# Performance work log

Hardware: AMD Instinct MI355X
Metric: run time of the kernel (lower is better)

Reference implementation:

```python
import jax, jax.numpy as jnp
import numpy as np
from jax import lax

B, T, N, H, NC = 2, 8, 512, 64, 10
NEG = -1e9
LN_EPS = 1e-5


def _gatv2(x, mask, Wl, Wr, att, b):
    # GATv2Conv (PyG semantics, eval mode): e_ij = att . leaky_relu(Wr x_i + Wl x_j),
    # softmax over source nodes j with self-loops, out_i = sum_j alpha_ij * (Wl x_j).
    # x: (B, N, Fin); mask: (N, N) bool adjacency incl. self-loops; att: (heads, C).
    heads, C = att.shape
    Bn, Nn, _ = x.shape
    xl = (x @ Wl).reshape(Bn, Nn, heads, C)  # source transform
    xr = (x @ Wr).reshape(Bn, Nn, heads, C)  # target transform
    s = jax.nn.leaky_relu(xr[:, :, None] + xl[:, None, :], 0.2)  # (B, Ni, Nj, h, C)
    e = jnp.einsum('bijhc,hc->bijh', s, att)
    e = jnp.where(mask[None, :, :, None], e, NEG)
    alpha = jax.nn.softmax(e, axis=2)  # softmax over neighbors j
    out = jnp.einsum('bijh,bjhc->bihc', alpha, xl)
    return out.reshape(Bn, Nn, heads * C) + b


def _gru_layer(x, Wih, Whh, bih, bhh):
    # torch nn.GRU single layer, batch_first; x: (B, T, Hin)
    h0 = jnp.zeros((x.shape[0], Whh.shape[0]), x.dtype)
    def step(h, xt):
        gi = xt @ Wih + bih
        gh = h @ Whh + bhh
        ir, iz, inn = jnp.split(gi, 3, axis=-1)
        hr, hz, hn = jnp.split(gh, 3, axis=-1)
        r = jax.nn.sigmoid(ir + hr)
        z = jax.nn.sigmoid(iz + hz)
        n = jnp.tanh(inn + r * hn)
        hnew = (1.0 - z) * n + z * h
        return hnew, hnew
    _, ys = lax.scan(step, h0, jnp.swapaxes(x, 0, 1))
    return jnp.swapaxes(ys, 0, 1)


def setup_inputs() -> dict:
    key = jax.random.key(0)
    ks = jax.random.split(key, 20)
    def rn(i, shape, s=0.1):
        return jax.random.normal(ks[i], shape, jnp.float32) * s
    x_seq = jax.random.normal(ks[0], (B, T, N, 1), jnp.float32)
    a = jax.random.uniform(ks[1], (N, N))
    up = jnp.triu((a > 0.95).astype(jnp.float32), 1)
    static_adj = up + up.T  # sparse symmetric 0/1 static graph
    dyn_W = jax.random.normal(ks[2], (N, N), jnp.float32)
    reg_lambda = jnp.array([0.05], jnp.float32)
    return {
        'x_seq': x_seq, 'static_adj': static_adj, 'dyn_W': dyn_W, 'reg_lambda': reg_lambda,
        'g1_Wl': rn(3, (1, H)), 'g1_Wr': rn(4, (1, H)), 'g1_att': rn(5, (4, H // 4)), 'g1_b': jnp.zeros(H),
        'g2_Wl': rn(6, (H, H)), 'g2_Wr': rn(7, (H, H)), 'g2_att': rn(8, (1, H)), 'g2_b': jnp.zeros(H),
        'gru_Wih0': rn(9, (H, 3 * H)), 'gru_Whh0': rn(10, (H, 3 * H)), 'gru_bih0': jnp.zeros(3 * H), 'gru_bhh0': jnp.zeros(3 * H),
        'gru_Wih1': rn(11, (H, 3 * H)), 'gru_Whh1': rn(12, (H, 3 * H)), 'gru_bih1': jnp.zeros(3 * H), 'gru_bhh1': jnp.zeros(3 * H),
        'attn_W': rn(13, (H, 1)), 'attn_b': jnp.zeros(1),
        'cls_W1': rn(14, (H, H)), 'cls_b1': jnp.zeros(H), 'ln_g': jnp.ones(H), 'ln_b': jnp.zeros(H),
        'cls_W2': rn(15, (H, NC)), 'cls_b2': jnp.zeros(NC),
    }


def reference(x_seq, static_adj, dyn_W, reg_lambda,
              g1_Wl, g1_Wr, g1_att, g1_b, g2_Wl, g2_Wr, g2_att, g2_b,
              gru_Wih0, gru_Whh0, gru_bih0, gru_bhh0,
              gru_Wih1, gru_Whh1, gru_bih1, gru_bhh1,
              attn_W, attn_b, cls_W1, cls_b1, ln_g, ln_b, cls_W2, cls_b2):
    Bn, Tn, Nn, _ = x_seq.shape
    lam = jnp.maximum(reg_lambda[0], 0.01)
    t = jnp.arange(Tn, dtype=x_seq.dtype)
    gts = jnp.exp(-lam * t)  # gating values per timestep
    dyn = jax.nn.relu(dyn_W + dyn_W.T)
    fused = gts[:, None, None] * static_adj + (1.0 - gts)[:, None, None] * dyn  # (T, N, N)
    masks = (fused > 0) | jnp.eye(Nn, dtype=bool)[None]  # edge set + self-loops

    def step(carry, inp):
        xt, mask = inp  # xt: (B, N, 1)
        h = jax.nn.elu(_gatv2(xt, mask, g1_Wl, g1_Wr, g1_att, g1_b))
        h = jax.nn.elu(_gatv2(h, mask, g2_Wl, g2_Wr, g2_att, g2_b))
        return carry, h.mean(axis=1)  # (B, H) graph readout

    _, reps = lax.scan(step, 0.0, (jnp.swapaxes(x_seq, 0, 1), masks))
    h_seq = jnp.swapaxes(reps, 0, 1)  # (B, T, H)

    gru_out = _gru_layer(h_seq, gru_Wih0, gru_Whh0, gru_bih0, gru_bhh0)
    gru_out = _gru_layer(gru_out, gru_Wih1, gru_Whh1, gru_bih1, gru_bhh1)

    att_scores = jax.nn.softmax((gru_out @ attn_W + attn_b)[..., 0], axis=1)  # (B, T)
    final = jnp.einsum('bt,bth->bh', att_scores, gru_out)

    z = final @ cls_W1 + cls_b1
    mu = jnp.mean(z, axis=-1, keepdims=True)
    var = jnp.var(z, axis=-1, keepdims=True)
    z = (z - mu) / jnp.sqrt(var + LN_EPS) * ln_g + ln_b
    z = jax.nn.gelu(z, approximate=False)
    logits = z @ cls_W2 + cls_b2
    return logits, gts, att_scores
```

## Files before the change

### kernel.cpp

```cpp
#include <hip/hip_runtime.h>
#include <math.h>

#define BB 2
#define TT 8
#define NN 512
#define HH 64
#define NC 10

typedef unsigned char uchar;

__device__ __forceinline__ float elu1(float v){ return v > 0.f ? v : expm1f(v); }
__device__ __forceinline__ float sigm(float v){ return 1.f/(1.f+expf(-v)); }

__global__ __launch_bounds__(256) void k_mask(
    const float* __restrict__ dW, const float* __restrict__ sadj,
    uchar* __restrict__ M0, uchar* __restrict__ M1,
    float* __restrict__ Z2, float* __restrict__ hseq,
    const float* __restrict__ att1, const float* __restrict__ Wr1,
    const float* __restrict__ Wl1, float* __restrict__ AB)
{
    __shared__ float tr[64][65];
    int bx = blockIdx.x, by = blockIdx.y;
    int i0 = by*64, j0 = bx*64;
    int tid = threadIdx.x;
    #pragma unroll
    for (int q = 0; q < 4; ++q){
        int r = (tid >> 4) + 16*q, c4 = tid & 15;
        float4 v = *(const float4*)&dW[(size_t)(j0+r)*NN + i0 + 4*c4];
        tr[r][4*c4+0] = v.x; tr[r][4*c4+1] = v.y;
        tr[r][4*c4+2] = v.z; tr[r][4*c4+3] = v.w;
    }
    __syncthreads();
    #pragma unroll
    for (int q = 0; q < 4; ++q){
        int row = (tid >> 4) + 16*q, c4 = tid & 15;
        int i = i0 + row, j = j0 + 4*c4;
        float4 d  = *(const float4*)&dW[(size_t)i*NN + j];
        float4 sa = *(const float4*)&sadj[(size_t)i*NN + j];
        uchar4 m0, m1;
        float dd0 = d.x + tr[4*c4+0][row];
        float dd1 = d.y + tr[4*c4+1][row];
        float dd2 = d.z + tr[4*c4+2][row];
        float dd3 = d.w + tr[4*c4+3][row];
        m0.x = (sa.x > 0.f) || (i == j+0);
        m0.y = (sa.y > 0.f) || (i == j+1);
        m0.z = (sa.z > 0.f) || (i == j+2);
        m0.w = (sa.w > 0.f) || (i == j+3);
        m1.x = m0.x || (dd0 > 0.f);
        m1.y = m0.y || (dd1 > 0.f);
        m1.z = m0.z || (dd2 > 0.f);
        m1.w = m0.w || (dd3 > 0.f);
        *(uchar4*)&M0[(size_t)i*NN + j] = m0;
        *(uchar4*)&M1[(size_t)i*NN + j] = m1;
    }
    int flat = (by*8 + bx)*256 + tid;
    if (flat < BB*TT*NN) Z2[flat] = 0.f;
    else if (flat < BB*TT*NN + BB*TT*HH) hseq[flat - BB*TT*NN] = 0.f;
    if (bx == 0 && by == 0 && tid < 8){
        int h = tid & 3;
        const float* W = (tid < 4) ? Wr1 : Wl1;
        float s = 0.f;
        for (int c = 0; c < 16; ++c) s += att1[h*16+c]*W[h*16+c];
        AB[tid] = s;
    }
}

__global__ __launch_bounds__(256) void k_gat1f(
    const float* __restrict__ x_seq, const uchar* __restrict__ M0,
    const uchar* __restrict__ M1,
    const float* __restrict__ Wl, const float* __restrict__ Wr,
    const float* __restrict__ att, const float* __restrict__ bias,
    const float* __restrict__ AB,
    const float* __restrict__ Wl2, const float* __restrict__ Wr2,
    const float* __restrict__ att2,
    float* __restrict__ xl2, float* __restrict__ xr2,
    float* __restrict__ ui, float* __restrict__ vj)
{
    __shared__ float x_s[NN];
    __shared__ float S_s[4][4];
    __shared__ float h_s[4][HH];
    __shared__ float Wl2_s[64*64];
    __shared__ float Wr2_s[64*64];
    int bt = blockIdx.y; int t = bt % TT;
    int i0 = blockIdx.x * 4;
    int tid = threadIdx.x;
    int il = tid >> 6, jl = tid & 63;
    int i = i0 + il;
    const uchar* M = t ? M1 : M0;
    ((float2*)x_s)[tid] = ((const float2*)(x_seq + bt*NN))[tid];
    #pragma unroll
    for (int q = 0; q < 4; ++q){
        int idx = q*256 + tid;
        ((float4*)Wl2_s)[idx] = ((const float4*)Wl2)[idx];
        ((float4*)Wr2_s)[idx] = ((const float4*)Wr2)[idx];
    }
    __syncthreads();
    float xi = x_s[i];
    const uchar* Mrow = M + (size_t)i*NN;
    float xj[8], msk[8];
    #pragma unroll
    for (int jj = 0; jj < 8; ++jj){
        int j = jj*64 + jl;
        xj[jj] = x_s[j];
        msk[jj] = Mrow[j] ? 1.f : 0.f;
    }
    float sw[4] = {0,0,0,0}, swx[4] = {0,0,0,0};
    for (int h = 0; h < 4; ++h){
        float acc[8] = {0,0,0,0,0,0,0,0};
        #pragma unroll
        for (int c = 0; c < 16; ++c){
            int hc = h*16 + c;
            float wl = Wl[hc];
            float q  = 0.4f * att[hc];
            float pr = xi * Wr[hc];
            #pragma unroll
            for (int jj = 0; jj < 8; ++jj){
                float s = fmaf(xj[jj], wl, pr);
                acc[jj] = fmaf(q, fabsf(s), acc[jj]);
            }
        }
        float lin = 0.6f * xi * AB[h];
        float al6 = 0.6f * AB[4+h];
        #pragma unroll
        for (int jj = 0; jj < 8; ++jj){
            float e = acc[jj] + fmaf(al6, xj[jj], lin);
            float w = msk[jj] * __expf(e);
            sw[h] += w;
            swx[h] = fmaf(w, xj[jj], swx[h]);
        }
    }
    #pragma unroll
    for (int off = 32; off; off >>= 1){
        #pragma unroll
        for (int h = 0; h < 4; ++h){
            sw[h]  += __shfl_down(sw[h],  off);
            swx[h] += __shfl_down(swx[h], off);
        }
    }
    if (jl == 0){
        #pragma unroll
        for (int h = 0; h < 4; ++h) S_s[il][h] = swx[h] / sw[h];
    }
    __syncthreads();
    {
        int hc = tid & 63, row = tid >> 6;
        float v = S_s[row][hc >> 4] * Wl[hc] + bias[hc];
        h_s[row][hc] = elu1(v);
    }
    __syncthreads();
    {
        int c = tid & 63, row = tid >> 6;
        float al = 0.f, ar = 0.f;
        #pragma unroll 8
        for (int k = 0; k < 64; ++k){
            float hv = h_s[row][k];
            al = fmaf(hv, Wl2_s[k*64 + c], al);
            ar = fmaf(hv, Wr2_s[k*64 + c], ar);
        }
        size_t ridx = (size_t)(bt*NN + i0 + row);
        xl2[ridx*HH + c] = al;
        xr2[ridx*HH + c] = ar;
        float a2 = att2[c];
        float pu = a2 * ar, pv = a2 * al;
        #pragma unroll
        for (int off = 32; off; off >>= 1){
            pu += __shfl_down(pu, off);
            pv += __shfl_down(pv, off);
        }
        if (c == 0){ ui[ridx] = pu; vj[ridx] = pv; }
    }
}

__global__ __launch_bounds__(256) void k_e2(
    const float* __restrict__ xl2, const float* __restrict__ xr2,
    const uchar* __restrict__ M0, const uchar* __restrict__ M1,
    const float* __restrict__ att,
    const float* __restrict__ ui, const float* __restrict__ vj,
    float* __restrict__ WgT, float* __restrict__ Z2)
{
    __shared__ float xrT[64][68];
    __shared__ float xlT[64][68];
    int bt = blockIdx.z, t = bt % TT;
    int i0 = blockIdx.y*64, j0 = blockIdx.x*64;
    int base = bt*NN;
    int tid = threadIdx.x;
    const uchar* M = t ? M1 : M0;
    {
        int r = tid >> 2;
        #pragma unroll
        for (int q = 0; q < 4; ++q){
            int c4 = (tid & 3) + 4*q;
            float4 a = *(const float4*)&xr2[(size_t)(base+i0+r)*HH + 4*c4];
            float4 b = *(const float4*)&xl2[(size_t)(base+j0+r)*HH + 4*c4];
            xrT[4*c4+0][r] = a.x; xrT[4*c4+1][r] = a.y;
            xrT[4*c4+2][r] = a.z; xrT[4*c4+3][r] = a.w;
            xlT[4*c4+0][r] = b.x; xlT[4*c4+1][r] = b.y;
            xlT[4*c4+2][r] = b.z; xlT[4*c4+3][r] = b.w;
        }
    }
    int ti = tid >> 4, tj = tid & 15;
    int iL = ti*4, jL = tj*4;
    float4 u4 = *(const float4*)&ui[base+i0+iL];
    float4 v4 = *(const float4*)&vj[base+j0+jL];
    float uu[4] = {u4.x, u4.y, u4.z, u4.w};
    float vv[4] = {v4.x, v4.y, v4.z, v4.w};
    float acc[4][4];
    #pragma unroll
    for (int ii = 0; ii < 4; ++ii)
        #pragma unroll
        for (int jj = 0; jj < 4; ++jj)
            acc[ii][jj] = 0.6f*(uu[ii] + vv[jj]);
    __syncthreads();
    #pragma unroll 8
    for (int c = 0; c < 64; ++c){
        float qa = 0.4f * att[c];
        float4 a4 = *(const float4*)&xrT[c][iL];
        float4 b4 = *(const float4*)&xlT[c][jL];
        float a[4] = {a4.x, a4.y, a4.z, a4.w};
        float b[4] = {b4.x, b4.y, b4.z, b4.w};
        #pragma unroll
        for (int ii = 0; ii < 4; ++ii)
            #pragma unroll
            for (int jj = 0; jj < 4; ++jj)
                acc[ii][jj] = fmaf(qa, fabsf(a[ii] + b[jj]), acc[ii][jj]);
    }
    float w[4][4];
    #pragma unroll
    for (int ii = 0; ii < 4; ++ii){
        int i = i0 + iL + ii;
        uchar4 mr = *(const uchar4*)&M[(size_t)i*NN + j0 + jL];
        w[ii][0] = mr.x ? __expf(acc[ii][0]) : 0.f;
        w[ii][1] = mr.y ? __expf(acc[ii][1]) : 0.f;
        w[ii][2] = mr.z ? __expf(acc[ii][2]) : 0.f;
        w[ii][3] = mr.w ? __expf(acc[ii][3]) : 0.f;
    }
    #pragma unroll
    for (int jj = 0; jj < 4; ++jj){
        int j = j0 + jL + jj;
        float4 wv = { w[0][jj], w[1][jj], w[2][jj], w[3][jj] };
        *(float4*)&WgT[(size_t)(base+j)*NN + i0 + iL] = wv;
    }
    #pragma unroll
    for (int ii = 0; ii < 4; ++ii){
        float zi = w[ii][0] + w[ii][1] + w[ii][2] + w[ii][3];
        zi += __shfl_down(zi, 8);
        zi += __shfl_down(zi, 4);
        zi += __shfl_down(zi, 2);
        zi += __shfl_down(zi, 1);
        if (tj == 0) atomicAdd(&Z2[base + i0 + iL + ii], zi);
    }
}

__global__ __launch_bounds__(256) void k_a2(
    const float* __restrict__ WgT, const float* __restrict__ xl2,
    const float* __restrict__ Z2, const float* __restrict__ bias,
    float* __restrict__ hseq)
{
    __shared__ float a_s[64][20];
    __shared__ float x_s[64][68];
    __shared__ float msum[64];
    int bt = blockIdx.y;
    int i0 = blockIdx.x * 16;
    int base = bt * NN;
    int tid = threadIdx.x;
    int tg = tid >> 4, tc = tid & 15;
    if (tid < 64) msum[tid] = 0.f;
    float4 acc = {0,0,0,0};
    for (int jc = 0; jc < 8; ++jc){
        int j0 = jc*64;
        {
            int row = tid >> 2, c4 = tid & 3;
            ((float4*)&a_s[row][0])[c4] = ((const float4*)&WgT[(size_t)(base+j0+row)*NN + i0])[c4];
        }
        #pragma unroll
        for (int q = 0; q < 4; ++q){
            int idx = q*256 + tid; int row = idx >> 4, c4 = idx & 15;
            ((float4*)&x_s[row][0])[c4] = ((const float4*)&xl2[(size_t)(base+j0+row)*HH])[c4];
        }
        __syncthreads();
        #pragma unroll 8
        for (int j = 0; j < 64; ++j){
            float a = a_s[j][tg];
            float4 xv = ((float4*)&x_s[j][0])[tc];
            acc.x = fmaf(a, xv.x, acc.x);
            acc.y = fmaf(a, xv.y, acc.y);
            acc.z = fmaf(a, xv.z, acc.z);
            acc.w = fmaf(a, xv.w, acc.w);
        }
        __syncthreads();
    }
    float rz = 1.f / Z2[base + i0 + tg];
    float4 b4 = ((const float4*)bias)[tc];
    float4 h;
    h.x = elu1(acc.x*rz + b4.x);
    h.y = elu1(acc.y*rz + b4.y);
    h.z = elu1(acc.z*rz + b4.z);
    h.w = elu1(acc.w*rz + b4.w);
    atomicAdd(&msum[tc*4+0], h.x);
    atomicAdd(&msum[tc*4+1], h.y);
    atomicAdd(&msum[tc*4+2], h.z);
    atomicAdd(&msum[tc*4+3], h.w);
    __syncthreads();
    if (tid < 64) atomicAdd(&hseq[bt*HH + tid], msum[tid]*(1.f/(float)NN));
}

__global__ __launch_bounds__(512) void k_gruhead(
    const float* __restrict__ hseq,
    const float* __restrict__ Wih0, const float* __restrict__ Whh0,
    const float* __restrict__ bih0, const float* __restrict__ bhh0,
    const float* __restrict__ Wih1, const float* __restrict__ Whh1,
    const float* __restrict__ bih1, const float* __restrict__ bhh1,
    const float* __restrict__ lamp, const float* __restrict__ attn_W,
    const float* __restrict__ attn_b, const float* __restrict__ W1,
    const float* __restrict__ b1, const float* __restrict__ ln_g,
    const float* __restrict__ ln_b, const float* __restrict__ W2,
    const float* __restrict__ b2, float* __restrict__ out)
{
    __shared__ float W_s[64*192];
    __shared__ float gi_s[BB*TT*192];
    __shared__ float x_s[BB*TT*HH];
    __shared__ float y_s[BB*TT*HH];
    __shared__ float h_s[BB][HH];
    __shared__ float gh_s[BB][192];
    __shared__ float sc_s[BB][TT], at_s[BB][TT];
    __shared__ float fin_s[BB][HH], z_s[BB][HH], g_s[BB][HH];
    __shared__ float mu_s[BB], iv_s[BB];
    int tid = threadIdx.x;
    int b = tid / 192, g = tid % 192;
    for (int k = tid; k < BB*TT*HH; k += 512) x_s[k] = hseq[k];
    for (int L = 0; L < 2; ++L){
        const float* Wih = L ? Wih1 : Wih0;
        const float* Whh = L ? Whh1 : Whh0;
        const float* bih = L ? bih1 : bih0;
        const float* bhh = L ? bhh1 : bhh0;
        __syncthreads();
        for (int k = tid; k < 64*192; k += 512) W_s[k] = Wih[k];
        __syncthreads();
        if (tid < 384){
            float accT[TT];
            #pragma unroll
            for (int t = 0; t < TT; ++t) accT[t] = bih[g];
            for (int k = 0; k < HH; ++k){
                float wk = W_s[k*192 + g];
                #pragma unroll
                for (int t = 0; t < TT; ++t)
                    accT[t] = fmaf(x_s[(b*TT+t)*HH + k], wk, accT[t]);
            }
            #pragma unroll
            for (int t = 0; t < TT; ++t) gi_s[(b*TT+t)*192 + g] = accT[t];
        }
        __syncthreads();
        for (int k = tid; k < 64*192; k += 512) W_s[k] = Whh[k];
        if (tid < BB*HH) h_s[tid>>6][tid&63] = 0.f;
        __syncthreads();
        for (int t = 0; t < TT; ++t){
            if (tid < 384){
                float gh = bhh[g];
                #pragma unroll 8
                for (int k = 0; k < HH; ++k)
                    gh = fmaf(h_s[b][k], W_s[k*192 + g], gh);
                gh_s[b][g] = gh;
            }
            __syncthreads();
            if (tid < BB*HH){
                int b2 = tid >> 6, gg = tid & 63;
                const float* gi = &gi_s[(b2*TT+t)*192];
                float r = sigm(gi[gg]      + gh_s[b2][gg]);
                float z = sigm(gi[64+gg]   + gh_s[b2][64+gg]);
                float n = tanhf(gi[128+gg] + r*gh_s[b2][128+gg]);
                float hn = (1.f - z)*n + z*h_s[b2][gg];
                h_s[b2][gg] = hn;
                y_s[(b2*TT + t)*HH + gg] = hn;
            }
            __syncthreads();
        }
        if (L == 0){
            for (int k = tid; k < BB*TT*HH; k += 512) x_s[k] = y_s[k];
        }
    }
    __syncthreads();
    float lam = fmaxf(lamp[0], 0.01f);
    if (tid < TT) out[BB*NC + tid] = expf(-lam*(float)tid);
    if (tid < BB*TT){
        int bb = tid >> 3, t = tid & 7;
        float s = attn_b[0];
        const float* r = &y_s[(bb*TT+t)*HH];
        for (int h = 0; h < HH; ++h) s += r[h]*attn_W[h];
        sc_s[bb][t] = s;
    }
    __syncthreads();
    if (tid < BB){
        float mx = -INFINITY;
        for (int t = 0; t < TT; ++t) mx = fmaxf(mx, sc_s[tid][t]);
        float se = 0.f;
        for (int t = 0; t < TT; ++t){ float w = expf(sc_s[tid][t]-mx); at_s[tid][t] = w; se += w; }
        for (int t = 0; t < TT; ++t){
            at_s[tid][t] /= se;
            out[BB*NC + TT + tid*TT + t] = at_s[tid][t];
        }
    }
    __syncthreads();
    if (tid < BB*HH){
        int bb = tid >> 6, h = tid & 63;
        float a = 0.f;
        for (int t = 0; t < TT; ++t) a += at_s[bb][t]*y_s[(bb*TT+t)*HH + h];
        fin_s[bb][h] = a;
    }
    __syncthreads();
    if (tid < BB*HH){
        int bb = tid >> 6, h = tid & 63;
        float a = b1[h];
        for (int k = 0; k < HH; ++k) a += fin_s[bb][k]*W1[k*HH+h];
        z_s[bb][h] = a;
    }
    __syncthreads();
    if (tid < BB){
        float mu = 0.f;
        for (int h = 0; h < HH; ++h) mu += z_s[tid][h];
        mu *= (1.f/HH);
        float v = 0.f;
        for (int h = 0; h < HH; ++h){ float d = z_s[tid][h]-mu; v += d*d; }
        v *= (1.f/HH);
        mu_s[tid] = mu; iv_s[tid] = 1.f/sqrtf(v + 1e-5f);
    }
    __syncthreads();
    if (tid < BB*HH){
        int bb = tid >> 6, h = tid & 63;
        float zn = (z_s[bb][h]-mu_s[bb])*iv_s[bb]*ln_g[h] + ln_b[h];
        g_s[bb][h] = 0.5f*zn*(1.f + erff(zn*0.70710678118654752f));
    }
    __syncthreads();
    if (tid < BB*NC){
        int bb = tid / NC, c = tid % NC;
        float a = b2[c];
        for (int k = 0; k < HH; ++k) a += g_s[bb][k]*W2[k*NC+c];
        out[bb*NC + c] = a;
    }
}

extern "C" void kernel_launch(void* const* d_in, const int* in_sizes, int n_in,
                              void* d_out, int out_size, void* d_ws, size_t ws_size,
                              hipStream_t stream)
{
    const float* x_seq = (const float*)d_in[0];
    const float* sadj  = (const float*)d_in[1];
    const float* dynW  = (const float*)d_in[2];
    const float* lamp  = (const float*)d_in[3];
    const float* g1_Wl = (const float*)d_in[4];
    const float* g1_Wr = (const float*)d_in[5];
    const float* g1_att= (const float*)d_in[6];
    const float* g1_b  = (const float*)d_in[7];
    const float* g2_Wl = (const float*)d_in[8];
    const float* g2_Wr = (const float*)d_in[9];
    const float* g2_att= (const float*)d_in[10];
    const float* g2_b  = (const float*)d_in[11];
    const float* Wih0  = (const float*)d_in[12];
    const float* Whh0  = (const float*)d_in[13];
    const float* bih0  = (const float*)d_in[14];
    const float* bhh0  = (const float*)d_in[15];
    const float* Wih1  = (const float*)d_in[16];
    const float* Whh1  = (const float*)d_in[17];
    const float* bih1  = (const float*)d_in[18];
    const float* bhh1  = (const float*)d_in[19];
    const float* attnW = (const float*)d_in[20];
    const float* attnb = (const float*)d_in[21];
    const float* W1    = (const float*)d_in[22];
    const float* b1    = (const float*)d_in[23];
    const float* lng   = (const float*)d_in[24];
    const float* lnb   = (const float*)d_in[25];
    const float* W2    = (const float*)d_in[26];
    const float* b2    = (const float*)d_in[27];
    float* out = (float*)d_out;

    const int RWS = BB*TT*NN*HH;
    uchar* M0 = (uchar*)d_ws;
    uchar* M1 = M0 + (size_t)NN*NN;
    float* fb = (float*)(M1 + (size_t)NN*NN);
    float* Z2   = fb;
    float* AB   = Z2   + BB*TT*NN;
    float* ui   = AB   + 16;
    float* vj   = ui   + BB*TT*NN;
    float* xl2  = vj   + BB*TT*NN;
    float* xr2  = xl2  + RWS;
    float* WgT  = xr2  + RWS;
    float* hseq = WgT  + (size_t)BB*TT*NN*NN;

    k_mask <<<dim3(8,8), 256, 0, stream>>>(dynW, sadj, M0, M1, Z2, hseq, g1_att, g1_Wr, g1_Wl, AB);
    k_gat1f<<<dim3(NN/4, BB*TT), 256, 0, stream>>>(x_seq, M0, M1, g1_Wl, g1_Wr, g1_att, g1_b, AB,
                                                   g2_Wl, g2_Wr, g2_att, xl2, xr2, ui, vj);
    k_e2   <<<dim3(NN/64, NN/64, BB*TT), 256, 0, stream>>>(xl2, xr2, M0, M1, g2_att, ui, vj, WgT, Z2);
    k_a2   <<<dim3(NN/16, BB*TT), 256, 0, stream>>>(WgT, xl2, Z2, g2_b, hseq);
    k_gruhead<<<1, 512, 0, stream>>>(hseq, Wih0, Whh0, bih0, bhh0, Wih1, Whh1, bih1, bhh1,
                                     lamp, attnW, attnb, W1, b1, lng, lnb, W2, b2, out);
}
```

Measured before the change: 226.1 us.

## Restructure GRU head into wave-level recurrence with shuffles and pre-transposed weights

The GRU weights are pre-transposed into gate-interleaved float4 layout inside extra blocks of the mask kernel. The layer-0 input projection moves to a separate small multi-block kernel. The recurrence now runs with one wave per batch element, keeping hidden state in registers and broadcasting it with shuffles, which removes the per-timestep block barriers and shared round trips. This adds an extra kernel launch and uses only two waves for the serial part, leaving most of the block idle.

Measured after the change: 223.0 us. Within noise of the previous version (-1.4%).

```diff
diff --git a/kernel.cpp b/kernel.cpp
--- a/kernel.cpp
+++ b/kernel.cpp
@@ -17,12 +17,29 @@
     uchar* __restrict__ M0, uchar* __restrict__ M1,
     float* __restrict__ Z2, float* __restrict__ hseq,
     const float* __restrict__ att1, const float* __restrict__ Wr1,
-    const float* __restrict__ Wl1, float* __restrict__ AB)
+    const float* __restrict__ Wl1, float* __restrict__ AB,
+    const float* __restrict__ Whh0, const float* __restrict__ Wih1,
+    const float* __restrict__ Whh1, float4* __restrict__ WT4)
 {
     __shared__ float tr[64][65];
     int bx = blockIdx.x, by = blockIdx.y;
+    int tid = threadIdx.x;
+    if (blockIdx.z == 1){
+        int idx = (by*8 + bx)*256 + tid;
+        if (idx < 3*4096){
+            int m = idx >> 12, r = idx & 4095;
+            int gg = r >> 6, k = r & 63;
+            const float* W = (m == 0) ? Whh0 : (m == 1) ? Wih1 : Whh1;
+            float4 o;
+            o.x = W[k*192 + gg];
+            o.y = W[k*192 + 64 + gg];
+            o.z = W[k*192 + 128 + gg];
+            o.w = 0.f;
+            WT4[(size_t)m*4096 + r] = o;
+        }
+        return;
+    }
     int i0 = by*64, j0 = bx*64;
-    int tid = threadIdx.x;
     #pragma unroll
     for (int q = 0; q < 4; ++q){
         int r = (tid >> 4) + 16*q, c4 = tid & 15;
@@ -304,11 +321,24 @@
     if (tid < 64) atomicAdd(&hseq[bt*HH + tid], msum[tid]*(1.f/(float)NN));
 }
 
-__global__ __launch_bounds__(512) void k_gruhead(
-    const float* __restrict__ hseq,
-    const float* __restrict__ Wih0, const float* __restrict__ Whh0,
-    const float* __restrict__ bih0, const float* __restrict__ bhh0,
-    const float* __restrict__ Wih1, const float* __restrict__ Whh1,
+__global__ __launch_bounds__(256) void k_pre(
+    const float* __restrict__ hseq, const float* __restrict__ Wih0,
+    const float* __restrict__ bih0, float* __restrict__ gi0)
+{
+    int idx = blockIdx.x*256 + threadIdx.x;
+    int bt = idx / 192, g = idx % 192;
+    const float* x = hseq + bt*HH;
+    float acc = bih0[g];
+    #pragma unroll 8
+    for (int k = 0; k < HH; ++k)
+        acc = fmaf(x[k], Wih0[k*192 + g], acc);
+    gi0[idx] = acc;
+}
+
+#define P4 65
+__global__ __launch_bounds__(512) void k_gru2(
+    const float* __restrict__ gi0, const float4* __restrict__ WT4,
+    const float* __restrict__ bhh0,
     const float* __restrict__ bih1, const float* __restrict__ bhh1,
     const float* __restrict__ lamp, const float* __restrict__ attn_W,
     const float* __restrict__ attn_b, const float* __restrict__ W1,
@@ -316,66 +346,84 @@
     const float* __restrict__ ln_b, const float* __restrict__ W2,
     const float* __restrict__ b2, float* __restrict__ out)
 {
-    __shared__ float W_s[64*192];
+    __shared__ float4 WA[64*P4];
+    __shared__ float4 WB[64*P4];
     __shared__ float gi_s[BB*TT*192];
-    __shared__ float x_s[BB*TT*HH];
     __shared__ float y_s[BB*TT*HH];
-    __shared__ float h_s[BB][HH];
-    __shared__ float gh_s[BB][192];
     __shared__ float sc_s[BB][TT], at_s[BB][TT];
     __shared__ float fin_s[BB][HH], z_s[BB][HH], g_s[BB][HH];
     __shared__ float mu_s[BB], iv_s[BB];
     int tid = threadIdx.x;
-    int b = tid / 192, g = tid % 192;
-    for (int k = tid; k < BB*TT*HH; k += 512) x_s[k] = hseq[k];
-    for (int L = 0; L < 2; ++L){
-        const float* Wih = L ? Wih1 : Wih0;
-        const float* Whh = L ? Whh1 : Whh0;
-        const float* bih = L ? bih1 : bih0;
-        const float* bhh = L ? bhh1 : bhh0;
-        __syncthreads();
-        for (int k = tid; k < 64*192; k += 512) W_s[k] = Wih[k];
-        __syncthreads();
-        if (tid < 384){
-            float accT[TT];
+    int wave = tid >> 6, lane = tid & 63;
+    for (int v = tid; v < 4096; v += 512){
+        WA[(v >> 6)*P4 + (v & 63)] = WT4[v];
+        WB[(v >> 6)*P4 + (v & 63)] = WT4[4096 + v];
+    }
+    for (int v = tid; v < BB*TT*192; v += 512) gi_s[v] = gi0[v];
+    __syncthreads();
+    float y[TT];
+    float g1r[TT], g1z[TT], g1n[TT];
+    if (wave < 2){
+        int b = wave;
+        float bhr = bhh0[lane], bhz = bhh0[64+lane], bhn = bhh0[128+lane];
+        float h = 0.f;
+        for (int t = 0; t < TT; ++t){
+            float ghr = bhr, ghz = bhz, ghn = bhn;
+            #pragma unroll 16
+            for (int k = 0; k < 64; ++k){
+                float4 w4 = WA[lane*P4 + k];
+                float hk = __shfl(h, k);
+                ghr = fmaf(w4.x, hk, ghr);
+                ghz = fmaf(w4.y, hk, ghz);
+                ghn = fmaf(w4.z, hk, ghn);
+            }
+            const float* gi = &gi_s[(b*TT + t)*192];
+            float r = sigm(gi[lane] + ghr);
+            float z = sigm(gi[64+lane] + ghz);
+            float n = tanhf(gi[128+lane] + r*ghn);
+            h = (1.f - z)*n + z*h;
+            y[t] = h;
+        }
+        float bi1r = bih1[lane], bi1z = bih1[64+lane], bi1n = bih1[128+lane];
+        #pragma unroll
+        for (int t = 0; t < TT; ++t){ g1r[t] = bi1r; g1z[t] = bi1z; g1n[t] = bi1n; }
+        #pragma unroll 8
+        for (int k = 0; k < 64; ++k){
+            float4 w4 = WB[lane*P4 + k];
             #pragma unroll
-            for (int t = 0; t < TT; ++t) accT[t] = bih[g];
-            for (int k = 0; k < HH; ++k){
-                float wk = W_s[k*192 + g];
-                #pragma unroll
-                for (int t = 0; t < TT; ++t)
-                    accT[t] = fmaf(x_s[(b*TT+t)*HH + k], wk, accT[t]);
+            for (int t = 0; t < TT; ++t){
+                float yk = __shfl(y[t], k);
+                g1r[t] = fmaf(w4.x, yk, g1r[t]);
+                g1z[t] = fmaf(w4.y, yk, g1z[t]);
+                g1n[t] = fmaf(w4.z, yk, g1n[t]);
             }
-            #pragma unroll
-            for (int t = 0; t < TT; ++t) gi_s[(b*TT+t)*192 + g] = accT[t];
-        }
-        __syncthreads();
-        for (int k = tid; k < 64*192; k += 512) W_s[k] = Whh[k];
-        if (tid < BB*HH) h_s[tid>>6][tid&63] = 0.f;
-        __syncthreads();
+        }
+    }
+    __syncthreads();
+    if (wave >= 2){
+        for (int v = tid - 128; v < 4096; v += 384)
+            WA[(v >> 6)*P4 + (v & 63)] = WT4[2*4096 + v];
+    }
+    __syncthreads();
+    if (wave < 2){
+        int b = wave;
+        float bhr = bhh1[lane], bhz = bhh1[64+lane], bhn = bhh1[128+lane];
+        float h = 0.f;
         for (int t = 0; t < TT; ++t){
-            if (tid < 384){
-                float gh = bhh[g];
-                #pragma unroll 8
-                for (int k = 0; k < HH; ++k)
-                    gh = fmaf(h_s[b][k], W_s[k*192 + g], gh);
-                gh_s[b][g] = gh;
+            float ghr = bhr, ghz = bhz, ghn = bhn;
+            #pragma unroll 16
+            for (int k = 0; k < 64; ++k){
+                float4 w4 = WA[lane*P4 + k];
+                float hk = __shfl(h, k);
+                ghr = fmaf(w4.x, hk, ghr);
+                ghz = fmaf(w4.y, hk, ghz);
+                ghn = fmaf(w4.z, hk, ghn);
             }
-            __syncthreads();
-            if (tid < BB*HH){
-                int b2 = tid >> 6, gg = tid & 63;
-                const float* gi = &gi_s[(b2*TT+t)*192];
-                float r = sigm(gi[gg]      + gh_s[b2][gg]);
-                float z = sigm(gi[64+gg]   + gh_s[b2][64+gg]);
-                float n = tanhf(gi[128+gg] + r*gh_s[b2][128+gg]);
-                float hn = (1.f - z)*n + z*h_s[b2][gg];
-                h_s[b2][gg] = hn;
-                y_s[(b2*TT + t)*HH + gg] = hn;
-            }
-            __syncthreads();
-        }
-        if (L == 0){
-            for (int k = tid; k < BB*TT*HH; k += 512) x_s[k] = y_s[k];
+            float r = sigm(g1r[t] + ghr);
+            float z = sigm(g1z[t] + ghz);
+            float n = tanhf(g1n[t] + r*ghn);
+            h = (1.f - z)*n + z*h;
+            y_s[(b*TT + t)*HH + lane] = h;
         }
     }
     __syncthreads();
@@ -484,12 +532,16 @@
     float* xr2  = xl2  + RWS;
     float* WgT  = xr2  + RWS;
     float* hseq = WgT  + (size_t)BB*TT*NN*NN;
-
-    k_mask <<<dim3(8,8), 256, 0, stream>>>(dynW, sadj, M0, M1, Z2, hseq, g1_att, g1_Wr, g1_Wl, AB);
+    float* gi0  = hseq + BB*TT*HH;
+    float4* WT4 = (float4*)(gi0 + BB*TT*192);
+
+    k_mask <<<dim3(8,8,2), 256, 0, stream>>>(dynW, sadj, M0, M1, Z2, hseq, g1_att, g1_Wr, g1_Wl, AB,
+                                             Whh0, Wih1, Whh1, WT4);
     k_gat1f<<<dim3(NN/4, BB*TT), 256, 0, stream>>>(x_seq, M0, M1, g1_Wl, g1_Wr, g1_att, g1_b, AB,
                                                    g2_Wl, g2_Wr, g2_att, xl2, xr2, ui, vj);
     k_e2   <<<dim3(NN/64, NN/64, BB*TT), 256, 0, stream>>>(xl2, xr2, M0, M1, g2_att, ui, vj, WgT, Z2);
     k_a2   <<<dim3(NN/16, BB*TT), 256, 0, stream>>>(WgT, xl2, Z2, g2_b, hseq);
-    k_gruhead<<<1, 512, 0, stream>>>(hseq, Wih0, Whh0, bih0, bhh0, Wih1, Whh1, bih1, bhh1,
-                                     lamp, attnW, attnb, W1, b1, lng, lnb, W2, b2, out);
-}
+    k_pre  <<<12, 256, 0, stream>>>(hseq, Wih0, bih0, gi0);
+    k_gru2 <<<1, 512, 0, stream>>>(gi0, WT4, bhh0, bih1, bhh1,
+                                   lamp, attnW, attnb, W1, b1, lng, lnb, W2, b2, out);
+}
```
